# Kernel tuning notes

Measured on AMD Instinct MI355X. Metric: run time of the kernel, lower is better.

Reference implementation:

```python
import jax, jax.numpy as jnp
import numpy as np

HEADS = 4
HEAD_DIM = 32
DIM = 256
HIDDEN = HEADS * HEAD_DIM  # 128
SCALE = HEAD_DIM ** -0.5


def rmsnorm(x, g):
    # channel-wise L2 normalize (dim=1) * g * sqrt(C), lucidrains-style RMSNorm for conv maps
    inv = jax.lax.rsqrt(jnp.sum(x * x, axis=1, keepdims=True) + 1e-12)
    return x * inv * (g * (x.shape[1] ** 0.5))[None, :, None, None]


def setup_inputs() -> dict:
    key = jax.random.key(0)
    k1, k2, k3 = jax.random.split(key, 3)
    b, H, W = 16, 64, 64
    x = jax.random.normal(k1, (b, DIM, H, W), dtype=jnp.float32)
    W_qkv = jax.random.normal(k2, (3 * HIDDEN, DIM), dtype=jnp.float32) * (DIM ** -0.5)
    W_out = jax.random.normal(k3, (DIM, HIDDEN), dtype=jnp.float32) * (HIDDEN ** -0.5)
    b_out = jnp.zeros((DIM,), dtype=jnp.float32)
    g_norm = jnp.ones((DIM,), dtype=jnp.float32)
    g_out = jnp.ones((DIM,), dtype=jnp.float32)
    return {"x": x, "W_qkv": W_qkv, "W_out": W_out, "b_out": b_out,
            "g_norm": g_norm, "g_out": g_out}


def reference(x, W_qkv, W_out, b_out, g_norm, g_out):
    b, c, H, W = x.shape
    n = H * W
    xn = rmsnorm(x, g_norm)
    # 1x1 conv projection to q,k,v: (b, 3*hidden, H, W)
    qkv = jnp.einsum('bchw,oc->bohw', xn, W_qkv)
    qkv = qkv.reshape(b, 3, HEADS, HEAD_DIM, n)
    q, k, v = qkv[:, 0], qkv[:, 1], qkv[:, 2]  # (b, h, d, n)
    q = jax.nn.softmax(q, axis=-2)  # over head_dim
    k = jax.nn.softmax(k, axis=-1)  # over tokens
    # context: (b, h, d, e)
    context = jnp.einsum('bhdn,bhen->bhde', k, v)
    out = jnp.einsum('bhde,bhdn->bhen', context, q) * SCALE  # (b, h, e, n)
    out = out.reshape(b, HIDDEN, H, W)
    out = jnp.einsum('bchw,oc->bohw', out, W_out) + b_out[None, :, None, None]
    return rmsnorm(out, g_out)
```

## Files before the change

### kernel.cpp

```cpp
#include <hip/hip_runtime.h>


typedef _Float16 half8 __attribute__((ext_vector_type(8)));
typedef _Float16 half4 __attribute__((ext_vector_type(4)));
typedef float f32x4 __attribute__((ext_vector_type(4)));

#define SCALE_F 0.17677669529663687f

__global__ __launch_bounds__(256) void kW(const float* __restrict__ W_qkv,
                                          const float* __restrict__ W_out,
                                          const float* __restrict__ g_norm,
                                          _Float16* __restrict__ W16,
                                          _Float16* __restrict__ Wo16) {
  const int t = threadIdx.x;
  __shared__ float g16s[256];
  g16s[t] = g_norm[t] * 16.0f;
  __syncthreads();
  #pragma unroll
  for (int i = 0; i < 8; ++i) {
    int idx = blockIdx.x * 2048 + i * 256 + t;
    if (idx < 24576) {
      f32x4 v = *(const f32x4*)(W_qkv + (size_t)idx * 4);
      int c0 = (idx & 63) * 4;
      half4 h = {(_Float16)(v[0] * g16s[c0]), (_Float16)(v[1] * g16s[c0 + 1]),
                 (_Float16)(v[2] * g16s[c0 + 2]), (_Float16)(v[3] * g16s[c0 + 3])};
      *(half4*)(W16 + (size_t)idx * 4) = h;
    } else {
      f32x4 v = *(const f32x4*)(W_out + (size_t)(idx - 24576) * 4);
      half4 h = {(_Float16)v[0], (_Float16)v[1], (_Float16)v[2], (_Float16)v[3]};
      *(half4*)(Wo16 + (size_t)(idx - 24576) * 4) = h;
    }
  }
}

#define LOAD_AF(dst, mtv)                                                            \
  {                                                                                  \
    const _Float16* Wm_ = W16 + (size_t)((mtv) * 128 + h * 32) * 256;                \
    _Pragma("unroll")                                                                \
    for (int ks = 0; ks < 8; ++ks)                                                   \
      _Pragma("unroll")                                                              \
      for (int mf = 0; mf < 2; ++mf)                                                 \
        dst[ks][mf] = *(const half8*)(Wm_ + (size_t)(mf * 16 + ll) * 256 +           \
                                      ks * 32 + lg * 8);                             \
  }

#define GEMM_PHASE(afc)                                                              \
  {                                                                                  \
    _Pragma("unroll")                                                                \
    for (int i = 0; i < 2; ++i)                                                      \
      _Pragma("unroll")                                                              \
      for (int j = 0; j < 4; ++j) acc[i][j] = fz;                                    \
    _Pragma("unroll")                                                                \
    for (int ks = 0; ks < 8; ++ks) {                                                 \
      half8 bf[4];                                                                   \
      _Pragma("unroll")                                                              \
      for (int nf = 0; nf < 4; ++nf)                                                 \
        bf[nf] = *(const half8*)(xbuf + (nf * 16 + ll) * 512 +                       \
                                 ((((ks * 4 + lg) ^ ll) ^ ((nf & 1) << 4)) << 4));   \
      _Pragma("unroll")                                                              \
      for (int mf = 0; mf < 2; ++mf)                                                 \
        _Pragma("unroll")                                                            \
        for (int nf = 0; nf < 4; ++nf)                                               \
          acc[mf][nf] =                                                              \
              __builtin_amdgcn_mfma_f32_16x16x32_f16(afc[ks][mf], bf[nf],            \
                                                     acc[mf][nf], 0, 0, 0);          \
    }                                                                                \
  }

__global__ __launch_bounds__(256, 3) void k2_mega(const _Float16* __restrict__ W16,
                                                  const float* __restrict__ x,
                                                  _Float16* __restrict__ qhat,
                                                  float* __restrict__ ctxp,
                                                  float* __restrict__ sumep) {
  const int pt = blockIdx.x, b = blockIdx.y;
  const int p0 = pt * 64;
  const int t = threadIdx.x;
  const int h = t >> 6, l = t & 63;
  const int lg = l >> 4, ll = l & 15;
  const int u = l & 3;
  __shared__ __align__(1024) char smem[50432];
  char* xbuf = smem;
  char* r2 = smem + 32768;
  char* vt = smem;
  float* psum = (float*)(smem + 49152);
  float* sinvp = (float*)(smem + 50176);

  f32x4 vx[16];
  const float* xb = x + ((size_t)(b * 256 + h * 64)) * 4096 + p0 + (l & ~3);
  #pragma unroll
  for (int it = 0; it < 16; ++it)
    vx[it] = *(const f32x4*)(xb + (size_t)(it * 4 + u) * 4096);
  half8 afA[8][2], afB[8][2];
  LOAD_AF(afA, 0);
  float rsum = 0.f;
  #pragma unroll
  for (int it = 0; it < 16; ++it) {
    f32x4 v = vx[it];
    float sA = __shfl_xor((u & 1) ? v[0] : v[1], 1);
    float sB = __shfl_xor((u & 1) ? v[2] : v[3], 1);
    float a0 = (u & 1) ? sA : v[0];
    float a1 = (u & 1) ? v[1] : sA;
    float a2 = (u & 1) ? sB : v[2];
    float a3 = (u & 1) ? v[3] : sB;
    float sC = __shfl_xor((u & 2) ? a0 : a2, 2);
    float sD = __shfl_xor((u & 2) ? a1 : a3, 2);
    float w0 = (u & 2) ? sC : a0;
    float w1 = (u & 2) ? sD : a1;
    float w2 = (u & 2) ? a2 : sC;
    float w3 = (u & 2) ? a3 : sD;
    half4 hv = {(_Float16)w0, (_Float16)w1, (_Float16)w2, (_Float16)w3};
    #pragma unroll
    for (int j = 0; j < 4; ++j) { float f = (float)hv[j]; rsum += f * f; }
    int c = h * 8 + (it >> 1);
    int swz = c ^ (l & 15) ^ (((l >> 4) & 1) << 4);
    *(half4*)(xbuf + l * 512 + (swz << 4) + (it & 1) * 8) = hv;
  }
  psum[l * 4 + h] = rsum;
  __syncthreads();
  if (t < 64)
    sinvp[t] = rsqrtf(psum[t * 4] + psum[t * 4 + 1] + psum[t * 4 + 2] + psum[t * 4 + 3] + 1e-12f);
  __syncthreads();
  float sv[4];
  #pragma unroll
  for (int nf = 0; nf < 4; ++nf) sv[nf] = sinvp[nf * 16 + ll];

  const f32x4 fz = {0.f, 0.f, 0.f, 0.f};
  f32x4 acc[2][4];

  GEMM_PHASE(afA);
  LOAD_AF(afB, 1);
  {
    float s[4] = {0.f, 0.f, 0.f, 0.f};
    #pragma unroll
    for (int mf = 0; mf < 2; ++mf)
      #pragma unroll
      for (int nf = 0; nf < 4; ++nf)
        #pragma unroll
        for (int rr = 0; rr < 4; ++rr) {
          float v = __expf(acc[mf][nf][rr] * sv[nf]);
          acc[mf][nf][rr] = v;
          s[nf] += v;
        }
    #pragma unroll
    for (int nf = 0; nf < 4; ++nf) {
      s[nf] += __shfl_xor(s[nf], 16);
      s[nf] += __shfl_xor(s[nf], 32);
      s[nf] = 1.0f / s[nf];
    }
    #pragma unroll
    for (int mf = 0; mf < 2; ++mf)
      #pragma unroll
      for (int nf = 0; nf < 4; ++nf) {
        int px = nf * 16 + ll;
        int cphys = (h * 4 + mf * 2 + (lg >> 1)) ^ (px & 15);
        half4 hv;
        #pragma unroll
        for (int rr = 0; rr < 4; ++rr) hv[rr] = (_Float16)(acc[mf][nf][rr] * s[nf]);
        *(half4*)(r2 + px * 256 + (cphys << 4) + (lg & 1) * 8) = hv;
      }
    __syncthreads();
    _Float16* qb = qhat + ((size_t)b * 4096 + p0) * 128;
    #pragma unroll
    for (int i = 0; i < 4; ++i) {
      int q = i * 256 + t;
      int px = q >> 4, g = q & 15;
      half8 hv = *(const half8*)(r2 + px * 256 + ((g ^ (px & 15)) << 4));
      *(half8*)(qb + (size_t)px * 128 + g * 8) = hv;
    }
    __syncthreads();
  }

  GEMM_PHASE(afB);
  LOAD_AF(afA, 2);
  {
    float rs[2][4];
    #pragma unroll
    for (int mf = 0; mf < 2; ++mf)
      #pragma unroll
      for (int rr = 0; rr < 4; ++rr) rs[mf][rr] = 0.f;
    #pragma unroll
    for (int mf = 0; mf < 2; ++mf)
      #pragma unroll
      for (int nf = 0; nf < 4; ++nf)
        #pragma unroll
        for (int rr = 0; rr < 4; ++rr) {
          float v = __expf(acc[mf][nf][rr] * sv[nf] - 10.f);
          acc[mf][nf][rr] = v;
          rs[mf][rr] += v;
        }
    #pragma unroll
    for (int mf = 0; mf < 2; ++mf)
      #pragma unroll
      for (int rr = 0; rr < 4; ++rr) {
        float v = rs[mf][rr];
        v += __shfl_xor(v, 1);
        v += __shfl_xor(v, 2);
        v += __shfl_xor(v, 4);
        v += __shfl_xor(v, 8);
        rs[mf][rr] = v;
      }
    if (ll == 0) {
      #pragma unroll
      for (int mf = 0; mf < 2; ++mf)
        #pragma unroll
        for (int rr = 0; rr < 4; ++rr)
          sumep[((size_t)b * 128 + h * 32 + mf * 16 + lg * 4 + rr) * 64 + pt] = rs[mf][rr];
    }
    #pragma unroll
    for (int mf = 0; mf < 2; ++mf)
      #pragma unroll
      for (int nf = 0; nf < 4; ++nf)
        #pragma unroll
        for (int rr = 0; rr < 4; ++rr) {
          int ch = h * 32 + mf * 16 + lg * 4 + rr;
          int px = nf * 16 + ll;
          *(_Float16*)(r2 + ch * 128 + (((px >> 3) ^ (ch & 7)) << 4) + (px & 7) * 2) =
              (_Float16)acc[mf][nf][rr];
        }
  }

  GEMM_PHASE(afA);
  {
    __syncthreads();
    #pragma unroll
    for (int mf = 0; mf < 2; ++mf)
      #pragma unroll
      for (int nf = 0; nf < 4; ++nf)
        #pragma unroll
        for (int rr = 0; rr < 4; ++rr) {
          int ch = h * 32 + mf * 16 + lg * 4 + rr;
          int px = nf * 16 + ll;
          *(_Float16*)(vt + ch * 128 + (((px >> 3) ^ (ch & 7)) << 4) + (px & 7) * 2) =
              (_Float16)(acc[mf][nf][rr] * sv[nf]);
        }
    f32x4 ca[2][2] = {{fz, fz}, {fz, fz}};
    #pragma unroll
    for (int ks2 = 0; ks2 < 2; ++ks2) {
      half8 a2[2], b2[2];
      #pragma unroll
      for (int ti = 0; ti < 2; ++ti) {
        int ra = h * 32 + ti * 16 + ll;
        int cc = (ks2 * 4 + lg) ^ (ra & 7);
        a2[ti] = *(const half8*)(r2 + ra * 128 + (cc << 4));
        b2[ti] = *(const half8*)(vt + ra * 128 + (cc << 4));
      }
      #pragma unroll
      for (int ti = 0; ti < 2; ++ti)
        #pragma unroll
        for (int tj = 0; tj < 2; ++tj)
          ca[ti][tj] = __builtin_amdgcn_mfma_f32_16x16x32_f16(a2[ti], b2[tj], ca[ti][tj], 0, 0, 0);
    }
    float* cp = ctxp + (size_t)(((b * 64 + pt) * 4) + h) * 1024;
    #pragma unroll
    for (int ti = 0; ti < 2; ++ti)
      #pragma unroll
      for (int tj = 0; tj < 2; ++tj)
        #pragma unroll
        for (int rr = 0; rr < 4; ++rr)
          cp[(ti * 16 + lg * 4 + rr) * 32 + tj * 16 + ll] = ca[ti][tj][rr];
  }
}

__global__ __launch_bounds__(256) void k3_reduce(const float* __restrict__ ctxp,
                                                 const float* __restrict__ sumep,
                                                 float* __restrict__ ctx,
                                                 float* __restrict__ sume) {
  const int sl = blockIdx.x, b = blockIdx.y;
  const int t = threadIdx.x;
  if (sl == 0 && t < 128) {
    float s = 0.f;
    const float* sp = sumep + ((size_t)b * 128 + t) * 64;
    #pragma unroll 8
    for (int pt = 0; pt < 64; ++pt) s += sp[pt];
    sume[b * 128 + t] = s;
  }
  float a = 0.f;
  const float* p = ctxp + (size_t)b * 64 * 4096 + sl * 256 + t;
  #pragma unroll 8
  for (int pt = 0; pt < 64; ++pt) a += p[(size_t)pt * 4096];
  ctx[(size_t)b * 4096 + sl * 256 + t] = a;
}

__global__ __launch_bounds__(256) void k4b_fold(const _Float16* __restrict__ Wo16,
                                                const float* __restrict__ ctx,
                                                const float* __restrict__ sumexp,
                                                _Float16* __restrict__ M) {
  const int mq = blockIdx.x, b = blockIdx.y;
  const int t = threadIdx.x;
  const int h = t >> 6, l = t & 63;
  const int m0 = mq * 64;
  const float* cb = ctx + (size_t)(b * 4 + h) * 1024;
  const float* sb = sumexp + b * 128 + h * 32;
  half8 bf[2];
  #pragma unroll
  for (int n0 = 0; n0 < 2; ++n0) {
    int d = n0 * 16 + (l & 15);
    float s = SCALE_F / sb[d];
    const float* ce = cb + d * 32 + (l >> 4) * 8;
    half8 hb;
    #pragma unroll
    for (int j = 0; j < 8; ++j) hb[j] = (_Float16)(ce[j] * s);
    bf[n0] = hb;
  }
  const f32x4 fz = {0.f, 0.f, 0.f, 0.f};
  _Float16* Mb = M + (size_t)(b * 256) * 128;
  #pragma unroll
  for (int mf = 0; mf < 4; ++mf) {
    int row = m0 + mf * 16 + (l & 15);
    half8 af = *(const half8*)(Wo16 + (size_t)row * 128 + h * 32 + (l >> 4) * 8);
    #pragma unroll
    for (int n0 = 0; n0 < 2; ++n0) {
      f32x4 c = __builtin_amdgcn_mfma_f32_16x16x32_f16(af, bf[n0], fz, 0, 0, 0);
      #pragma unroll
      for (int rr = 0; rr < 4; ++rr) {
        int r = m0 + mf * 16 + (l >> 4) * 4 + rr;
        Mb[(size_t)r * 128 + h * 32 + n0 * 16 + (l & 15)] = (_Float16)c[rr];
      }
    }
  }
}

__global__ __launch_bounds__(256) void k5c_out(const _Float16* __restrict__ M,
                                               const _Float16* __restrict__ qhat,
                                               const float* __restrict__ b_out,
                                               const float* __restrict__ g_out,
                                               float* __restrict__ out) {
  const int pt = blockIdx.x, b = blockIdx.y;
  const int p0 = pt * 64;
  const int t = threadIdx.x;
  const int wid = t >> 6, l = t & 63;
  __shared__ __align__(16) char smem[81920];
  float* rp = (float*)smem;
  float* bo = (float*)(smem + 69632);
  float* g16o = (float*)(smem + 70656);
  float* psum = (float*)(smem + 71680);
  float* sinvp = (float*)(smem + 72704);
  const _Float16* Mb = M + (size_t)b * 256 * 128;
  const _Float16* Qb = qhat + ((size_t)b * 4096 + p0) * 128;
  #pragma unroll
  for (int i = 0; i < 16; ++i) {
    int ci = t + 256 * i;
    int r = ci >> 4, c = ci & 15;
    *(half8*)(smem + r * 256 + ((c ^ (r & 15)) << 4)) = *(const half8*)(Mb + (size_t)r * 128 + c * 8);
  }
  #pragma unroll
  for (int i = 0; i < 4; ++i) {
    int ci = t + 256 * i;
    int r = ci >> 4, c = ci & 15;
    *(half8*)(smem + 65536 + r * 256 + ((c ^ (r & 15)) << 4)) = *(const half8*)(Qb + (size_t)r * 128 + c * 8);
  }
  __syncthreads();
  const f32x4 fz = {0.f, 0.f, 0.f, 0.f};
  f32x4 acc[4][4];
  #pragma unroll
  for (int i = 0; i < 4; ++i)
    #pragma unroll
    for (int j = 0; j < 4; ++j) acc[i][j] = fz;
  #pragma unroll
  for (int kk = 0; kk < 4; ++kk) {
    half8 af[4], bf[4];
    int ck = kk * 4 + (l >> 4);
    #pragma unroll
    for (int mf = 0; mf < 4; ++mf) {
      int r = wid * 64 + mf * 16 + (l & 15);
      af[mf] = *(const half8*)(smem + r * 256 + ((ck ^ (r & 15)) << 4));
    }
    #pragma unroll
    for (int nf = 0; nf < 4; ++nf) {
      int r = nf * 16 + (l & 15);
      bf[nf] = *(const half8*)(smem + 65536 + r * 256 + ((ck ^ (r & 15)) << 4));
    }
    #pragma unroll
    for (int mf = 0; mf < 4; ++mf)
      #pragma unroll
      for (int nf = 0; nf < 4; ++nf)
        acc[mf][nf] = __builtin_amdgcn_mfma_f32_16x16x32_f16(af[mf], bf[nf], acc[mf][nf], 0, 0, 0);
  }
  __syncthreads();
  bo[t] = b_out[t];
  g16o[t] = g_out[t] * 16.0f;
  #pragma unroll
  for (int mf = 0; mf < 4; ++mf)
    #pragma unroll
    for (int nf = 0; nf < 4; ++nf)
      #pragma unroll
      for (int rr = 0; rr < 4; ++rr) {
        int r = wid * 64 + mf * 16 + (l >> 4) * 4 + rr;
        int px = nf * 16 + (l & 15);
        rp[r * 68 + px] = acc[mf][nf][rr];
      }
  __syncthreads();
  {
    int px = t & 63, q = t >> 6;
    float s = 0.f;
    #pragma unroll
    for (int i = 0; i < 64; ++i) {
      int r = q * 64 + i;
      float f = rp[r * 68 + px] + bo[r];
      s += f * f;
    }
    psum[px * 4 + q] = s;
  }
  __syncthreads();
  if (t < 64)
    sinvp[t] = rsqrtf(psum[t * 4] + psum[t * 4 + 1] + psum[t * 4 + 2] + psum[t * 4 + 3] + 1e-12f);
  __syncthreads();
  float* ob = out + (size_t)(b * 256) * 4096 + p0;
  #pragma unroll
  for (int i = 0; i < 16; ++i) {
    int idx4 = t + 256 * i;
    int r = idx4 >> 4, px4 = (idx4 & 15) * 4;
    f32x4 v;
    #pragma unroll
    for (int ii = 0; ii < 4; ++ii)
      v[ii] = (rp[r * 68 + px4 + ii] + bo[r]) * sinvp[px4 + ii] * g16o[r];
    *(f32x4*)(ob + (size_t)r * 4096 + px4) = v;
  }
}

extern "C" void kernel_launch(void* const* d_in, const int* in_sizes, int n_in,
                              void* d_out, int out_size, void* d_ws, size_t ws_size,
                              hipStream_t stream) {
  const float* x      = (const float*)d_in[0];
  const float* W_qkv  = (const float*)d_in[1];
  const float* W_out  = (const float*)d_in[2];
  const float* b_out  = (const float*)d_in[3];
  const float* g_norm = (const float*)d_in[4];
  const float* g_out  = (const float*)d_in[5];
  float* out = (float*)d_out;
  char* ws = (char*)d_ws;
  if (ws_size < 35659776) return;

  _Float16* W16   = (_Float16*)(ws);
  _Float16* Wo16  = (_Float16*)(ws + 196608);
  _Float16* qhat  = (_Float16*)(ws + 262144);
  float*    ctx   = (float*)(ws + 17039360);
  float*    sume  = (float*)(ws + 17301504);
  _Float16* M     = (_Float16*)(ws + 17309696);
  float*    ctxp  = (float*)(ws + 18358272);
  float*    sumep = (float*)(ws + 35135488);

  kW<<<16, 256, 0, stream>>>(W_qkv, W_out, g_norm, W16, Wo16);
  k2_mega<<<dim3(64, 16), 256, 0, stream>>>(W16, x, qhat, ctxp, sumep);
  k3_reduce<<<dim3(16, 16), 256, 0, stream>>>(ctxp, sumep, ctx, sume);
  k4b_fold<<<dim3(4, 16), 256, 0, stream>>>(Wo16, ctx, sume, M);
  k5c_out<<<dim3(64, 16), 256, 0, stream>>>(M, qhat, b_out, g_out, out);
}
```

Measured before the change: 77.86 us.

## Restructure QKV kernel: pixel-tiled waves with x fragments in registers, W streamed

The fused QKV/context kernel now gives each block 128 pixels and each wave 32 pixels. The normalized x fragments stay in registers as the MFMA A operand, and weights stream from global/L2 per output tile. The RMS norm is now computed per wave with shuffles, which removes the LDS staging of x and two block barriers. Query softmax results are written straight to global memory, and only k/v are staged in LDS for the context MFMA. Grid and partial-reduction counts are halved, at the cost of more per-wave global weight reads, lower occupancy (launch bounds 2) and scattered 2-byte qhat stores.

```diff
diff --git a/kernel.cpp b/kernel.cpp
--- a/kernel.cpp
+++ b/kernel.cpp
@@ -33,216 +33,166 @@
   }
 }
 
-#define LOAD_AF(dst, mtv)                                                            \
-  {                                                                                  \
-    const _Float16* Wm_ = W16 + (size_t)((mtv) * 128 + h * 32) * 256;                \
-    _Pragma("unroll")                                                                \
-    for (int ks = 0; ks < 8; ++ks)                                                   \
-      _Pragma("unroll")                                                              \
-      for (int mf = 0; mf < 2; ++mf)                                                 \
-        dst[ks][mf] = *(const half8*)(Wm_ + (size_t)(mf * 16 + ll) * 256 +           \
-                                      ks * 32 + lg * 8);                             \
-  }
-
-#define GEMM_PHASE(afc)                                                              \
-  {                                                                                  \
-    _Pragma("unroll")                                                                \
-    for (int i = 0; i < 2; ++i)                                                      \
-      _Pragma("unroll")                                                              \
-      for (int j = 0; j < 4; ++j) acc[i][j] = fz;                                    \
-    _Pragma("unroll")                                                                \
-    for (int ks = 0; ks < 8; ++ks) {                                                 \
-      half8 bf[4];                                                                   \
-      _Pragma("unroll")                                                              \
-      for (int nf = 0; nf < 4; ++nf)                                                 \
-        bf[nf] = *(const half8*)(xbuf + (nf * 16 + ll) * 512 +                       \
-                                 ((((ks * 4 + lg) ^ ll) ^ ((nf & 1) << 4)) << 4));   \
-      _Pragma("unroll")                                                              \
-      for (int mf = 0; mf < 2; ++mf)                                                 \
-        _Pragma("unroll")                                                            \
-        for (int nf = 0; nf < 4; ++nf)                                               \
-          acc[mf][nf] =                                                              \
-              __builtin_amdgcn_mfma_f32_16x16x32_f16(afc[ks][mf], bf[nf],            \
-                                                     acc[mf][nf], 0, 0, 0);          \
-    }                                                                                \
-  }
-
-__global__ __launch_bounds__(256, 3) void k2_mega(const _Float16* __restrict__ W16,
+__global__ __launch_bounds__(256, 2) void k2_mega(const _Float16* __restrict__ W16,
                                                   const float* __restrict__ x,
                                                   _Float16* __restrict__ qhat,
                                                   float* __restrict__ ctxp,
                                                   float* __restrict__ sumep) {
   const int pt = blockIdx.x, b = blockIdx.y;
-  const int p0 = pt * 64;
+  const int p0 = pt * 128;
   const int t = threadIdx.x;
-  const int h = t >> 6, l = t & 63;
+  const int w = t >> 6, l = t & 63;
   const int lg = l >> 4, ll = l & 15;
   const int u = l & 3;
-  __shared__ __align__(1024) char smem[50432];
-  char* xbuf = smem;
-  char* r2 = smem + 32768;
-  char* vt = smem;
-  float* psum = (float*)(smem + 49152);
-  float* sinvp = (float*)(smem + 50176);
-
-  f32x4 vx[16];
-  const float* xb = x + ((size_t)(b * 256 + h * 64)) * 4096 + p0 + (l & ~3);
-  #pragma unroll
-  for (int it = 0; it < 16; ++it)
-    vx[it] = *(const f32x4*)(xb + (size_t)(it * 4 + u) * 4096);
-  half8 afA[8][2], afB[8][2];
-  LOAD_AF(afA, 0);
-  float rsum = 0.f;
-  #pragma unroll
-  for (int it = 0; it < 16; ++it) {
-    f32x4 v = vx[it];
-    float sA = __shfl_xor((u & 1) ? v[0] : v[1], 1);
-    float sB = __shfl_xor((u & 1) ? v[2] : v[3], 1);
-    float a0 = (u & 1) ? sA : v[0];
-    float a1 = (u & 1) ? v[1] : sA;
-    float a2 = (u & 1) ? sB : v[2];
-    float a3 = (u & 1) ? v[3] : sB;
-    float sC = __shfl_xor((u & 2) ? a0 : a2, 2);
-    float sD = __shfl_xor((u & 2) ? a1 : a3, 2);
-    float w0 = (u & 2) ? sC : a0;
-    float w1 = (u & 2) ? sD : a1;
-    float w2 = (u & 2) ? a2 : sC;
-    float w3 = (u & 2) ? a3 : sD;
-    half4 hv = {(_Float16)w0, (_Float16)w1, (_Float16)w2, (_Float16)w3};
-    #pragma unroll
-    for (int j = 0; j < 4; ++j) { float f = (float)hv[j]; rsum += f * f; }
-    int c = h * 8 + (it >> 1);
-    int swz = c ^ (l & 15) ^ (((l >> 4) & 1) << 4);
-    *(half4*)(xbuf + l * 512 + (swz << 4) + (it & 1) * 8) = hv;
-  }
-  psum[l * 4 + h] = rsum;
-  __syncthreads();
-  if (t < 64)
-    sinvp[t] = rsqrtf(psum[t * 4] + psum[t * 4 + 1] + psum[t * 4 + 2] + psum[t * 4 + 3] + 1e-12f);
-  __syncthreads();
-  float sv[4];
-  #pragma unroll
-  for (int nf = 0; nf < 4; ++nf) sv[nf] = sinvp[nf * 16 + ll];
+  __shared__ __align__(1024) char smem[67584];
+  char* wt = smem;
+  char* vt = smem + 32768;
+  float* sums = (float*)(smem + 65536);
+
+  half8 af[2][8];
+  #pragma unroll
+  for (int s = 0; s < 2; ++s) {
+    const float* xb = x + ((size_t)b * 256) * 4096 + p0 + (2 * w + s) * 16 + ((l >> 2) & 3) * 4;
+    f32x4 tx[16];
+    #pragma unroll
+    for (int it = 0; it < 16; ++it) {
+      int ch = 32 * (it >> 1) + 8 * lg + 4 * (it & 1) + u;
+      f32x4 v = *(const f32x4*)(xb + (size_t)ch * 4096);
+      float sA = __shfl_xor((u & 1) ? v[0] : v[1], 1);
+      float sB = __shfl_xor((u & 1) ? v[2] : v[3], 1);
+      float a0 = (u & 1) ? sA : v[0];
+      float a1 = (u & 1) ? v[1] : sA;
+      float a2 = (u & 1) ? sB : v[2];
+      float a3 = (u & 1) ? v[3] : sB;
+      float sC = __shfl_xor((u & 2) ? a0 : a2, 2);
+      float sD = __shfl_xor((u & 2) ? a1 : a3, 2);
+      f32x4 o;
+      o[0] = (u & 2) ? sC : a0;
+      o[1] = (u & 2) ? sD : a1;
+      o[2] = (u & 2) ? a2 : sC;
+      o[3] = (u & 2) ? a3 : sD;
+      tx[it] = o;
+    }
+    float rs = 0.f;
+    #pragma unroll
+    for (int it = 0; it < 16; ++it)
+      #pragma unroll
+      for (int j = 0; j < 4; ++j) rs += tx[it][j] * tx[it][j];
+    rs += __shfl_xor(rs, 16);
+    rs += __shfl_xor(rs, 32);
+    float sinv = rsqrtf(rs + 1e-12f);
+    #pragma unroll
+    for (int ks = 0; ks < 8; ++ks) {
+      half8 hv;
+      #pragma unroll
+      for (int j = 0; j < 8; ++j)
+        hv[j] = (_Float16)(tx[ks * 2 + (j >> 2)][j & 3] * sinv);
+      af[s][ks] = hv;
+    }
+  }
 
   const f32x4 fz = {0.f, 0.f, 0.f, 0.f};
-  f32x4 acc[2][4];
-
-  GEMM_PHASE(afA);
-  LOAD_AF(afB, 1);
-  {
-    float s[4] = {0.f, 0.f, 0.f, 0.f};
-    #pragma unroll
-    for (int mf = 0; mf < 2; ++mf)
-      #pragma unroll
-      for (int nf = 0; nf < 4; ++nf)
-        #pragma unroll
-        for (int rr = 0; rr < 4; ++rr) {
-          float v = __expf(acc[mf][nf][rr] * sv[nf]);
-          acc[mf][nf][rr] = v;
-          s[nf] += v;
-        }
-    #pragma unroll
-    for (int nf = 0; nf < 4; ++nf) {
-      s[nf] += __shfl_xor(s[nf], 16);
-      s[nf] += __shfl_xor(s[nf], 32);
-      s[nf] = 1.0f / s[nf];
-    }
-    #pragma unroll
-    for (int mf = 0; mf < 2; ++mf)
-      #pragma unroll
-      for (int nf = 0; nf < 4; ++nf) {
-        int px = nf * 16 + ll;
-        int cphys = (h * 4 + mf * 2 + (lg >> 1)) ^ (px & 15);
-        half4 hv;
-        #pragma unroll
-        for (int rr = 0; rr < 4; ++rr) hv[rr] = (_Float16)(acc[mf][nf][rr] * s[nf]);
-        *(half4*)(r2 + px * 256 + (cphys << 4) + (lg & 1) * 8) = hv;
-      }
-    __syncthreads();
-    _Float16* qb = qhat + ((size_t)b * 4096 + p0) * 128;
-    #pragma unroll
-    for (int i = 0; i < 4; ++i) {
-      int q = i * 256 + t;
-      int px = q >> 4, g = q & 15;
-      half8 hv = *(const half8*)(r2 + px * 256 + ((g ^ (px & 15)) << 4));
-      *(half8*)(qb + (size_t)px * 128 + g * 8) = hv;
-    }
-    __syncthreads();
-  }
-
-  GEMM_PHASE(afB);
-  LOAD_AF(afA, 2);
-  {
-    float rs[2][4];
-    #pragma unroll
-    for (int mf = 0; mf < 2; ++mf)
-      #pragma unroll
-      for (int rr = 0; rr < 4; ++rr) rs[mf][rr] = 0.f;
-    #pragma unroll
-    for (int mf = 0; mf < 2; ++mf)
-      #pragma unroll
-      for (int nf = 0; nf < 4; ++nf)
-        #pragma unroll
-        for (int rr = 0; rr < 4; ++rr) {
-          float v = __expf(acc[mf][nf][rr] * sv[nf] - 10.f);
-          acc[mf][nf][rr] = v;
-          rs[mf][rr] += v;
-        }
-    #pragma unroll
-    for (int mf = 0; mf < 2; ++mf)
+  _Float16* qb = qhat + ((size_t)b * 4096 + p0) * 128;
+
+  #pragma unroll
+  for (int j = 0; j < 4; ++j) {
+    f32x4 a0[2] = {fz, fz}, a1[2] = {fz, fz};
+    #pragma unroll
+    for (int ks = 0; ks < 8; ++ks) {
+      half8 b0 = *(const half8*)(W16 + (size_t)(j * 32 + ll) * 256 + ks * 32 + lg * 8);
+      half8 b1 = *(const half8*)(W16 + (size_t)(j * 32 + 16 + ll) * 256 + ks * 32 + lg * 8);
+      #pragma unroll
+      for (int s = 0; s < 2; ++s) {
+        a0[s] = __builtin_amdgcn_mfma_f32_16x16x32_f16(af[s][ks], b0, a0[s], 0, 0, 0);
+        a1[s] = __builtin_amdgcn_mfma_f32_16x16x32_f16(af[s][ks], b1, a1[s], 0, 0, 0);
+      }
+    }
+    #pragma unroll
+    for (int s = 0; s < 2; ++s) {
+      float e0[4], e1[4], inv[4];
       #pragma unroll
       for (int rr = 0; rr < 4; ++rr) {
-        float v = rs[mf][rr];
+        e0[rr] = __expf(a0[s][rr]);
+        e1[rr] = __expf(a1[s][rr]);
+        float v = e0[rr] + e1[rr];
         v += __shfl_xor(v, 1);
         v += __shfl_xor(v, 2);
         v += __shfl_xor(v, 4);
         v += __shfl_xor(v, 8);
-        rs[mf][rr] = v;
-      }
-    if (ll == 0) {
-      #pragma unroll
-      for (int mf = 0; mf < 2; ++mf)
-        #pragma unroll
-        for (int rr = 0; rr < 4; ++rr)
-          sumep[((size_t)b * 128 + h * 32 + mf * 16 + lg * 4 + rr) * 64 + pt] = rs[mf][rr];
-    }
-    #pragma unroll
-    for (int mf = 0; mf < 2; ++mf)
-      #pragma unroll
-      for (int nf = 0; nf < 4; ++nf)
-        #pragma unroll
-        for (int rr = 0; rr < 4; ++rr) {
-          int ch = h * 32 + mf * 16 + lg * 4 + rr;
-          int px = nf * 16 + ll;
-          *(_Float16*)(r2 + ch * 128 + (((px >> 3) ^ (ch & 7)) << 4) + (px & 7) * 2) =
-              (_Float16)acc[mf][nf][rr];
-        }
-  }
-
-  GEMM_PHASE(afA);
+        inv[rr] = 1.0f / v;
+      }
+      #pragma unroll
+      for (int rr = 0; rr < 4; ++rr) {
+        int px = (2 * w + s) * 16 + lg * 4 + rr;
+        qb[(size_t)px * 128 + j * 32 + ll]      = (_Float16)(e0[rr] * inv[rr]);
+        qb[(size_t)px * 128 + j * 32 + 16 + ll] = (_Float16)(e1[rr] * inv[rr]);
+      }
+    }
+  }
+
+  #pragma unroll
+  for (int m = 0; m < 8; ++m) {
+    f32x4 a[2] = {fz, fz};
+    #pragma unroll
+    for (int ks = 0; ks < 8; ++ks) {
+      half8 bw = *(const half8*)(W16 + (size_t)(128 + m * 16 + ll) * 256 + ks * 32 + lg * 8);
+      #pragma unroll
+      for (int s = 0; s < 2; ++s)
+        a[s] = __builtin_amdgcn_mfma_f32_16x16x32_f16(af[s][ks], bw, a[s], 0, 0, 0);
+    }
+    int row = m * 16 + ll;
+    float part = 0.f;
+    #pragma unroll
+    for (int s = 0; s < 2; ++s) {
+      half4 hv;
+      #pragma unroll
+      for (int rr = 0; rr < 4; ++rr) {
+        float e = __expf(a[s][rr] - 10.f);
+        part += e;
+        hv[rr] = (_Float16)e;
+      }
+      int c = (2 * w + s) * 2 + (lg >> 1);
+      *(half4*)(wt + row * 256 + ((c ^ (row & 15)) << 4) + (lg & 1) * 8) = hv;
+    }
+    part += __shfl_xor(part, 16);
+    part += __shfl_xor(part, 32);
+    if (lg == 0) sums[row * 4 + w] = part;
+  }
+
+  #pragma unroll
+  for (int m = 0; m < 8; ++m) {
+    f32x4 a[2] = {fz, fz};
+    #pragma unroll
+    for (int ks = 0; ks < 8; ++ks) {
+      half8 bw = *(const half8*)(W16 + (size_t)(256 + m * 16 + ll) * 256 + ks * 32 + lg * 8);
+      #pragma unroll
+      for (int s = 0; s < 2; ++s)
+        a[s] = __builtin_amdgcn_mfma_f32_16x16x32_f16(af[s][ks], bw, a[s], 0, 0, 0);
+    }
+    int row = m * 16 + ll;
+    #pragma unroll
+    for (int s = 0; s < 2; ++s) {
+      half4 hv;
+      #pragma unroll
+      for (int rr = 0; rr < 4; ++rr) hv[rr] = (_Float16)a[s][rr];
+      int c = (2 * w + s) * 2 + (lg >> 1);
+      *(half4*)(vt + row * 256 + ((c ^ (row & 15)) << 4) + (lg & 1) * 8) = hv;
+    }
+  }
+
+  __syncthreads();
+
   {
-    __syncthreads();
-    #pragma unroll
-    for (int mf = 0; mf < 2; ++mf)
-      #pragma unroll
-      for (int nf = 0; nf < 4; ++nf)
-        #pragma unroll
-        for (int rr = 0; rr < 4; ++rr) {
-          int ch = h * 32 + mf * 16 + lg * 4 + rr;
-          int px = nf * 16 + ll;
-          *(_Float16*)(vt + ch * 128 + (((px >> 3) ^ (ch & 7)) << 4) + (px & 7) * 2) =
-              (_Float16)(acc[mf][nf][rr] * sv[nf]);
-        }
     f32x4 ca[2][2] = {{fz, fz}, {fz, fz}};
     #pragma unroll
-    for (int ks2 = 0; ks2 < 2; ++ks2) {
+    for (int ks2 = 0; ks2 < 4; ++ks2) {
       half8 a2[2], b2[2];
       #pragma unroll
       for (int ti = 0; ti < 2; ++ti) {
-        int ra = h * 32 + ti * 16 + ll;
-        int cc = (ks2 * 4 + lg) ^ (ra & 7);
-        a2[ti] = *(const half8*)(r2 + ra * 128 + (cc << 4));
-        b2[ti] = *(const half8*)(vt + ra * 128 + (cc << 4));
+        int row = w * 32 + ti * 16 + ll;
+        int c = (ks2 * 4 + lg) ^ (row & 15);
+        a2[ti] = *(const half8*)(wt + row * 256 + (c << 4));
+        b2[ti] = *(const half8*)(vt + row * 256 + (c << 4));
       }
       #pragma unroll
       for (int ti = 0; ti < 2; ++ti)
@@ -250,7 +200,7 @@
         for (int tj = 0; tj < 2; ++tj)
           ca[ti][tj] = __builtin_amdgcn_mfma_f32_16x16x32_f16(a2[ti], b2[tj], ca[ti][tj], 0, 0, 0);
     }
-    float* cp = ctxp + (size_t)(((b * 64 + pt) * 4) + h) * 1024;
+    float* cp = ctxp + (size_t)(((b * 32 + pt) * 4) + w) * 1024;
     #pragma unroll
     for (int ti = 0; ti < 2; ++ti)
       #pragma unroll
@@ -258,6 +208,14 @@
         #pragma unroll
         for (int rr = 0; rr < 4; ++rr)
           cp[(ti * 16 + lg * 4 + rr) * 32 + tj * 16 + ll] = ca[ti][tj][rr];
+    if (lg == 0) {
+      #pragma unroll
+      for (int ti = 0; ti < 2; ++ti) {
+        int ch = w * 32 + ti * 16 + ll;
+        float s4 = sums[ch * 4] + sums[ch * 4 + 1] + sums[ch * 4 + 2] + sums[ch * 4 + 3];
+        sumep[((size_t)b * 128 + ch) * 32 + pt] = s4;
+      }
+    }
   }
 }
 
@@ -269,15 +227,15 @@
   const int t = threadIdx.x;
   if (sl == 0 && t < 128) {
     float s = 0.f;
-    const float* sp = sumep + ((size_t)b * 128 + t) * 64;
+    const float* sp = sumep + ((size_t)b * 128 + t) * 32;
     #pragma unroll 8
-    for (int pt = 0; pt < 64; ++pt) s += sp[pt];
+    for (int pt = 0; pt < 32; ++pt) s += sp[pt];
     sume[b * 128 + t] = s;
   }
   float a = 0.f;
-  const float* p = ctxp + (size_t)b * 64 * 4096 + sl * 256 + t;
+  const float* p = ctxp + (size_t)b * 32 * 4096 + sl * 256 + t;
   #pragma unroll 8
-  for (int pt = 0; pt < 64; ++pt) a += p[(size_t)pt * 4096];
+  for (int pt = 0; pt < 32; ++pt) a += p[(size_t)pt * 4096];
   ctx[(size_t)b * 4096 + sl * 256 + t] = a;
 }
 
@@ -441,7 +399,7 @@
   float*    sumep = (float*)(ws + 35135488);
 
   kW<<<16, 256, 0, stream>>>(W_qkv, W_out, g_norm, W16, Wo16);
-  k2_mega<<<dim3(64, 16), 256, 0, stream>>>(W16, x, qhat, ctxp, sumep);
+  k2_mega<<<dim3(32, 16), 256, 0, stream>>>(W16, x, qhat, ctxp, sumep);
   k3_reduce<<<dim3(16, 16), 256, 0, stream>>>(ctxp, sumep, ctx, sume);
   k4b_fold<<<dim3(4, 16), 256, 0, stream>>>(Wo16, ctx, sume, M);
   k5c_out<<<dim3(64, 16), 256, 0, stream>>>(M, qhat, b_out, g_out, out);
```

Result: slower. 99.22 us (+27.4%).

## Halve k2 pixel tile to 32 and double grid, raising occupancy

Applied to the files above, without the earlier changes.

Halves the pixel tile of the fused QKV-projection kernel from 64 to 32 and doubles its grid to 128x16 blocks. Shared memory drops and launch bounds rise to 4 blocks per CU, and a single weight-fragment buffer replaces the double buffer to free registers. The x-load mapping, the LDS layouts and the context MFMA (now a single k-step) are reworked to match. In exchange, the per-tile partial context and sum-exp buffers double, so the reduction kernel reads twice as many partials and the workspace grows.

```diff
diff --git a/kernel.cpp b/kernel.cpp
--- a/kernel.cpp
+++ b/kernel.cpp
@@ -49,53 +49,55 @@
     _Pragma("unroll")                                                                \
     for (int i = 0; i < 2; ++i)                                                      \
       _Pragma("unroll")                                                              \
-      for (int j = 0; j < 4; ++j) acc[i][j] = fz;                                    \
+      for (int j = 0; j < 2; ++j) acc[i][j] = fz;                                    \
     _Pragma("unroll")                                                                \
     for (int ks = 0; ks < 8; ++ks) {                                                 \
-      half8 bf[4];                                                                   \
+      half8 bf[2];                                                                   \
       _Pragma("unroll")                                                              \
-      for (int nf = 0; nf < 4; ++nf)                                                 \
+      for (int nf = 0; nf < 2; ++nf)                                                 \
         bf[nf] = *(const half8*)(xbuf + (nf * 16 + ll) * 512 +                       \
-                                 ((((ks * 4 + lg) ^ ll) ^ ((nf & 1) << 4)) << 4));   \
+                                 ((((ks * 4 + lg) ^ ll) ^ (nf << 4)) << 4));         \
       _Pragma("unroll")                                                              \
       for (int mf = 0; mf < 2; ++mf)                                                 \
         _Pragma("unroll")                                                            \
-        for (int nf = 0; nf < 4; ++nf)                                               \
+        for (int nf = 0; nf < 2; ++nf)                                               \
           acc[mf][nf] =                                                              \
               __builtin_amdgcn_mfma_f32_16x16x32_f16(afc[ks][mf], bf[nf],            \
                                                      acc[mf][nf], 0, 0, 0);          \
     }                                                                                \
   }
 
-__global__ __launch_bounds__(256, 3) void k2_mega(const _Float16* __restrict__ W16,
+__global__ __launch_bounds__(256, 4) void k2_mega(const _Float16* __restrict__ W16,
                                                   const float* __restrict__ x,
                                                   _Float16* __restrict__ qhat,
                                                   float* __restrict__ ctxp,
                                                   float* __restrict__ sumep) {
   const int pt = blockIdx.x, b = blockIdx.y;
-  const int p0 = pt * 64;
+  const int p0 = pt * 32;
   const int t = threadIdx.x;
   const int h = t >> 6, l = t & 63;
   const int lg = l >> 4, ll = l & 15;
-  const int u = l & 3;
-  __shared__ __align__(1024) char smem[50432];
+  const int u = l & 3, pq = (l >> 2) & 7, hi = l >> 5;
+  __shared__ __align__(1024) char smem[37504];
   char* xbuf = smem;
-  char* r2 = smem + 32768;
-  char* vt = smem;
-  float* psum = (float*)(smem + 49152);
-  float* sinvp = (float*)(smem + 50176);
-
-  f32x4 vx[16];
-  const float* xb = x + ((size_t)(b * 256 + h * 64)) * 4096 + p0 + (l & ~3);
-  #pragma unroll
-  for (int it = 0; it < 16; ++it)
-    vx[it] = *(const f32x4*)(xb + (size_t)(it * 4 + u) * 4096);
-  half8 afA[8][2], afB[8][2];
-  LOAD_AF(afA, 0);
+  char* r2 = smem + 16384;
+  char* vt = smem + 26624;
+  float* psum = (float*)(smem + 36864);
+  float* sinvp = (float*)(smem + 37376);
+
+  f32x4 tx[8];
+  const float* xb = x + ((size_t)b * 256) * 4096 + p0 + pq * 4;
+  #pragma unroll
+  for (int it = 0; it < 8; ++it) {
+    int ch = h * 64 + it * 8 + hi * 4 + u;
+    tx[it] = *(const f32x4*)(xb + (size_t)ch * 4096);
+  }
+  half8 af[8][2];
+  LOAD_AF(af, 0);
   float rsum = 0.f;
   #pragma unroll
-  for (int it = 0; it < 16; ++it) {
-    f32x4 v = vx[it];
+  for (int it = 0; it < 8; ++it) {
+    f32x4 v = tx[it];
     float sA = __shfl_xor((u & 1) ? v[0] : v[1], 1);
     float sB = __shfl_xor((u & 1) ? v[2] : v[3], 1);
     float a0 = (u & 1) ? sA : v[0];
@@ -111,30 +113,32 @@
     half4 hv = {(_Float16)w0, (_Float16)w1, (_Float16)w2, (_Float16)w3};
     #pragma unroll
     for (int j = 0; j < 4; ++j) { float f = (float)hv[j]; rsum += f * f; }
-    int c = h * 8 + (it >> 1);
-    int swz = c ^ (l & 15) ^ (((l >> 4) & 1) << 4);
-    *(half4*)(xbuf + l * 512 + (swz << 4) + (it & 1) * 8) = hv;
-  }
-  psum[l * 4 + h] = rsum;
-  __syncthreads();
-  if (t < 64)
+    int px = pq * 4 + u;
+    int c = h * 8 + it;
+    int swz = c ^ (px & 15) ^ (((px >> 4) & 1) << 4);
+    *(half4*)(xbuf + px * 512 + (swz << 4) + hi * 8) = hv;
+  }
+  rsum += __shfl_xor(rsum, 32);
+  if (l < 32) psum[l * 4 + h] = rsum;
+  __syncthreads();
+  if (t < 32)
     sinvp[t] = rsqrtf(psum[t * 4] + psum[t * 4 + 1] + psum[t * 4 + 2] + psum[t * 4 + 3] + 1e-12f);
   __syncthreads();
-  float sv[4];
-  #pragma unroll
-  for (int nf = 0; nf < 4; ++nf) sv[nf] = sinvp[nf * 16 + ll];
+  float sv[2];
+  #pragma unroll
+  for (int nf = 0; nf < 2; ++nf) sv[nf] = sinvp[nf * 16 + ll];
 
   const f32x4 fz = {0.f, 0.f, 0.f, 0.f};
-  f32x4 acc[2][4];
-
-  GEMM_PHASE(afA);
-  LOAD_AF(afB, 1);
+  f32x4 acc[2][2];
+
+  GEMM_PHASE(af);
+  LOAD_AF(af, 1);
   {
-    float s[4] = {0.f, 0.f, 0.f, 0.f};
-    #pragma unroll
-    for (int mf = 0; mf < 2; ++mf)
-      #pragma unroll
-      for (int nf = 0; nf < 4; ++nf)
+    float s[2] = {0.f, 0.f};
+    #pragma unroll
+    for (int mf = 0; mf < 2; ++mf)
+      #pragma unroll
+      for (int nf = 0; nf < 2; ++nf)
         #pragma unroll
         for (int rr = 0; rr < 4; ++rr) {
           float v = __expf(acc[mf][nf][rr] * sv[nf]);
@@ -142,7 +146,7 @@
           s[nf] += v;
         }
     #pragma unroll
-    for (int nf = 0; nf < 4; ++nf) {
+    for (int nf = 0; nf < 2; ++nf) {
       s[nf] += __shfl_xor(s[nf], 16);
       s[nf] += __shfl_xor(s[nf], 32);
       s[nf] = 1.0f / s[nf];
@@ -150,7 +154,7 @@
     #pragma unroll
     for (int mf = 0; mf < 2; ++mf)
       #pragma unroll
-      for (int nf = 0; nf < 4; ++nf) {
+      for (int nf = 0; nf < 2; ++nf) {
         int px = nf * 16 + ll;
         int cphys = (h * 4 + mf * 2 + (lg >> 1)) ^ (px & 15);
         half4 hv;
@@ -161,7 +165,7 @@
     __syncthreads();
     _Float16* qb = qhat + ((size_t)b * 4096 + p0) * 128;
     #pragma unroll
-    for (int i = 0; i < 4; ++i) {
+    for (int i = 0; i < 2; ++i) {
       int q = i * 256 + t;
       int px = q >> 4, g = q & 15;
       half8 hv = *(const half8*)(r2 + px * 256 + ((g ^ (px & 15)) << 4));
@@ -170,8 +174,8 @@
     __syncthreads();
   }
 
-  GEMM_PHASE(afB);
-  LOAD_AF(afA, 2);
+  GEMM_PHASE(af);
+  LOAD_AF(af, 2);
   {
     float rs[2][4];
     #pragma unroll
@@ -181,7 +185,7 @@
     #pragma unroll
     for (int mf = 0; mf < 2; ++mf)
       #pragma unroll
-      for (int nf = 0; nf < 4; ++nf)
+      for (int nf = 0; nf < 2; ++nf)
         #pragma unroll
         for (int rr = 0; rr < 4; ++rr) {
           float v = __expf(acc[mf][nf][rr] * sv[nf] - 10.f);
@@ -204,53 +208,46 @@
       for (int mf = 0; mf < 2; ++mf)
         #pragma unroll
         for (int rr = 0; rr < 4; ++rr)
-          sumep[((size_t)b * 128 + h * 32 + mf * 16 + lg * 4 + rr) * 64 + pt] = rs[mf][rr];
-    }
-    #pragma unroll
-    for (int mf = 0; mf < 2; ++mf)
-      #pragma unroll
-      for (int nf = 0; nf < 4; ++nf)
+          sumep[((size_t)b * 128 + h * 32 + mf * 16 + lg * 4 + rr) * 128 + pt] = rs[mf][rr];
+    }
+    #pragma unroll
+    for (int mf = 0; mf < 2; ++mf)
+      #pragma unroll
+      for (int nf = 0; nf < 2; ++nf)
         #pragma unroll
         for (int rr = 0; rr < 4; ++rr) {
           int ch = h * 32 + mf * 16 + lg * 4 + rr;
           int px = nf * 16 + ll;
-          *(_Float16*)(r2 + ch * 128 + (((px >> 3) ^ (ch & 7)) << 4) + (px & 7) * 2) =
-              (_Float16)acc[mf][nf][rr];
+          *(_Float16*)(r2 + ch * 80 + px * 2) = (_Float16)acc[mf][nf][rr];
         }
   }
 
-  GEMM_PHASE(afA);
+  GEMM_PHASE(af);
   {
-    __syncthreads();
-    #pragma unroll
-    for (int mf = 0; mf < 2; ++mf)
-      #pragma unroll
-      for (int nf = 0; nf < 4; ++nf)
+    #pragma unroll
+    for (int mf = 0; mf < 2; ++mf)
+      #pragma unroll
+      for (int nf = 0; nf < 2; ++nf)
         #pragma unroll
         for (int rr = 0; rr < 4; ++rr) {
           int ch = h * 32 + mf * 16 + lg * 4 + rr;
           int px = nf * 16 + ll;
-          *(_Float16*)(vt + ch * 128 + (((px >> 3) ^ (ch & 7)) << 4) + (px & 7) * 2) =
-              (_Float16)(acc[mf][nf][rr] * sv[nf]);
+          *(_Float16*)(vt + ch * 80 + px * 2) = (_Float16)(acc[mf][nf][rr] * sv[nf]);
         }
-    f32x4 ca[2][2] = {{fz, fz}, {fz, fz}};
-    #pragma unroll
-    for (int ks2 = 0; ks2 < 2; ++ks2) {
-      half8 a2[2], b2[2];
-      #pragma unroll
-      for (int ti = 0; ti < 2; ++ti) {
-        int ra = h * 32 + ti * 16 + ll;
-        int cc = (ks2 * 4 + lg) ^ (ra & 7);
-        a2[ti] = *(const half8*)(r2 + ra * 128 + (cc << 4));
-        b2[ti] = *(const half8*)(vt + ra * 128 + (cc << 4));
-      }
-      #pragma unroll
-      for (int ti = 0; ti < 2; ++ti)
-        #pragma unroll
-        for (int tj = 0; tj < 2; ++tj)
-          ca[ti][tj] = __builtin_amdgcn_mfma_f32_16x16x32_f16(a2[ti], b2[tj], ca[ti][tj], 0, 0, 0);
-    }
-    float* cp = ctxp + (size_t)(((b * 64 + pt) * 4) + h) * 1024;
+    f32x4 ca[2][2];
+    half8 a2[2], b2[2];
+    #pragma unroll
+    for (int ti = 0; ti < 2; ++ti) {
+      int row = h * 32 + ti * 16 + ll;
+      a2[ti] = *(const half8*)(r2 + row * 80 + lg * 16);
+      b2[ti] = *(const half8*)(vt + row * 80 + lg * 16);
+    }
+    #pragma unroll
+    for (int ti = 0; ti < 2; ++ti)
+      #pragma unroll
+      for (int tj = 0; tj < 2; ++tj)
+        ca[ti][tj] = __builtin_amdgcn_mfma_f32_16x16x32_f16(a2[ti], b2[tj], fz, 0, 0, 0);
+    float* cp = ctxp + (size_t)(((b * 128 + pt) * 4) + h) * 1024;
     #pragma unroll
     for (int ti = 0; ti < 2; ++ti)
       #pragma unroll
@@ -269,15 +266,15 @@
   const int t = threadIdx.x;
   if (sl == 0 && t < 128) {
     float s = 0.f;
-    const float* sp = sumep + ((size_t)b * 128 + t) * 64;
+    const float* sp = sumep + ((size_t)b * 128 + t) * 128;
     #pragma unroll 8
-    for (int pt = 0; pt < 64; ++pt) s += sp[pt];
+    for (int pt = 0; pt < 128; ++pt) s += sp[pt];
     sume[b * 128 + t] = s;
   }
   float a = 0.f;
-  const float* p = ctxp + (size_t)b * 64 * 4096 + sl * 256 + t;
+  const float* p = ctxp + (size_t)b * 128 * 4096 + sl * 256 + t;
   #pragma unroll 8
-  for (int pt = 0; pt < 64; ++pt) a += p[(size_t)pt * 4096];
+  for (int pt = 0; pt < 128; ++pt) a += p[(size_t)pt * 4096];
   ctx[(size_t)b * 4096 + sl * 256 + t] = a;
 }
 
@@ -429,7 +426,7 @@
   const float* g_out  = (const float*)d_in[5];
   float* out = (float*)d_out;
   char* ws = (char*)d_ws;
-  if (ws_size < 35659776) return;
+  if (ws_size < 52961280) return;
 
   _Float16* W16   = (_Float16*)(ws);
   _Float16* Wo16  = (_Float16*)(ws + 196608);
@@ -438,10 +435,10 @@
   float*    sume  = (float*)(ws + 17301504);
   _Float16* M     = (_Float16*)(ws + 17309696);
   float*    ctxp  = (float*)(ws + 18358272);
-  float*    sumep = (float*)(ws + 35135488);
+  float*    sumep = (float*)(ws + 51912704);
 
   kW<<<16, 256, 0, stream>>>(W_qkv, W_out, g_norm, W16, Wo16);
-  k2_mega<<<dim3(64, 16), 256, 0, stream>>>(W16, x, qhat, ctxp, sumep);
+  k2_mega<<<dim3(128, 16), 256, 0, stream>>>(W16, x, qhat, ctxp, sumep);
   k3_reduce<<<dim3(16, 16), 256, 0, stream>>>(ctxp, sumep, ctx, sume);
   k4b_fold<<<dim3(4, 16), 256, 0, stream>>>(Wo16, ctx, sume, M);
   k5c_out<<<dim3(64, 16), 256, 0, stream>>>(M, qhat, b_out, g_out, out);
```

Measured after the change: 104.1 us. 1.34x slower.

## Fuse partial-context reduction into fold kernel and write q directly to global

Applied to the files above, without the earlier changes.

Merges the k3 reduction of per-tile context/sum partials into the k4b fold kernel, so each (head,batch) block reduces its own slice into shared memory before the MFMA fold. This drops one launch and the ctx/sume round trip through global memory. In k2_mega the q-hat output is now stored straight from registers as half4 writes instead of being staged through shared memory with two barriers, and each thread computes the rsqrt normalization itself rather than going through an extra barrier. The risks are less coalesced q stores and a reduction spread over only 64 blocks, which cuts parallelism for the 16 MB ctxp read.

```diff
diff --git a/kernel.cpp b/kernel.cpp
--- a/kernel.cpp
+++ b/kernel.cpp
@@ -78,12 +78,11 @@
   const int h = t >> 6, l = t & 63;
   const int lg = l >> 4, ll = l & 15;
   const int u = l & 3;
-  __shared__ __align__(1024) char smem[50432];
+  __shared__ __align__(1024) char smem[50176];
   char* xbuf = smem;
-  char* r2 = smem + 32768;
+  char* wt = smem + 32768;
   char* vt = smem;
   float* psum = (float*)(smem + 49152);
-  float* sinvp = (float*)(smem + 50176);
 
   f32x4 vx[16];
   const float* xb = x + ((size_t)(b * 256 + h * 64)) * 4096 + p0 + (l & ~3);
@@ -117,12 +116,13 @@
   }
   psum[l * 4 + h] = rsum;
   __syncthreads();
-  if (t < 64)
-    sinvp[t] = rsqrtf(psum[t * 4] + psum[t * 4 + 1] + psum[t * 4 + 2] + psum[t * 4 + 3] + 1e-12f);
-  __syncthreads();
   float sv[4];
   #pragma unroll
-  for (int nf = 0; nf < 4; ++nf) sv[nf] = sinvp[nf * 16 + ll];
+  for (int nf = 0; nf < 4; ++nf) {
+    int px = nf * 16 + ll;
+    sv[nf] = rsqrtf(psum[px * 4] + psum[px * 4 + 1] + psum[px * 4 + 2] +
+                    psum[px * 4 + 3] + 1e-12f);
+  }
 
   const f32x4 fz = {0.f, 0.f, 0.f, 0.f};
   f32x4 acc[2][4];
@@ -147,27 +147,17 @@
       s[nf] += __shfl_xor(s[nf], 32);
       s[nf] = 1.0f / s[nf];
     }
+    _Float16* qb = qhat + ((size_t)b * 4096 + p0) * 128 + h * 32 + lg * 4;
     #pragma unroll
     for (int mf = 0; mf < 2; ++mf)
       #pragma unroll
       for (int nf = 0; nf < 4; ++nf) {
         int px = nf * 16 + ll;
-        int cphys = (h * 4 + mf * 2 + (lg >> 1)) ^ (px & 15);
         half4 hv;
         #pragma unroll
         for (int rr = 0; rr < 4; ++rr) hv[rr] = (_Float16)(acc[mf][nf][rr] * s[nf]);
-        *(half4*)(r2 + px * 256 + (cphys << 4) + (lg & 1) * 8) = hv;
+        *(half4*)(qb + (size_t)px * 128 + mf * 16) = hv;
       }
-    __syncthreads();
-    _Float16* qb = qhat + ((size_t)b * 4096 + p0) * 128;
-    #pragma unroll
-    for (int i = 0; i < 4; ++i) {
-      int q = i * 256 + t;
-      int px = q >> 4, g = q & 15;
-      half8 hv = *(const half8*)(r2 + px * 256 + ((g ^ (px & 15)) << 4));
-      *(half8*)(qb + (size_t)px * 128 + g * 8) = hv;
-    }
-    __syncthreads();
   }
 
   GEMM_PHASE(afB);
@@ -214,7 +204,7 @@
         for (int rr = 0; rr < 4; ++rr) {
           int ch = h * 32 + mf * 16 + lg * 4 + rr;
           int px = nf * 16 + ll;
-          *(_Float16*)(r2 + ch * 128 + (((px >> 3) ^ (ch & 7)) << 4) + (px & 7) * 2) =
+          *(_Float16*)(wt + ch * 128 + (((px >> 3) ^ (ch & 7)) << 4) + (px & 7) * 2) =
               (_Float16)acc[mf][nf][rr];
         }
   }
@@ -241,7 +231,7 @@
       for (int ti = 0; ti < 2; ++ti) {
         int ra = h * 32 + ti * 16 + ll;
         int cc = (ks2 * 4 + lg) ^ (ra & 7);
-        a2[ti] = *(const half8*)(r2 + ra * 128 + (cc << 4));
+        a2[ti] = *(const half8*)(wt + ra * 128 + (cc << 4));
         b2[ti] = *(const half8*)(vt + ra * 128 + (cc << 4));
       }
       #pragma unroll
@@ -261,42 +251,40 @@
   }
 }
 
-__global__ __launch_bounds__(256) void k3_reduce(const float* __restrict__ ctxp,
-                                                 const float* __restrict__ sumep,
-                                                 float* __restrict__ ctx,
-                                                 float* __restrict__ sume) {
-  const int sl = blockIdx.x, b = blockIdx.y;
+__global__ __launch_bounds__(256) void k34(const float* __restrict__ ctxp,
+                                           const float* __restrict__ sumep,
+                                           const _Float16* __restrict__ Wo16,
+                                           _Float16* __restrict__ M) {
+  const int h = blockIdx.x, b = blockIdx.y;
   const int t = threadIdx.x;
-  if (sl == 0 && t < 128) {
+  __shared__ float ctx_s[1024];
+  __shared__ float sis[32];
+  {
+    f32x4 a = {0.f, 0.f, 0.f, 0.f};
+    const float* p = ctxp + ((size_t)(b * 64) * 4 + h) * 1024 + t * 4;
+    #pragma unroll 8
+    for (int pt = 0; pt < 64; ++pt) {
+      f32x4 v = *(const f32x4*)(p + (size_t)pt * 4096);
+      a[0] += v[0]; a[1] += v[1]; a[2] += v[2]; a[3] += v[3];
+    }
+    *(f32x4*)(ctx_s + t * 4) = a;
+  }
+  if (t < 32) {
     float s = 0.f;
-    const float* sp = sumep + ((size_t)b * 128 + t) * 64;
+    const float* sp = sumep + ((size_t)b * 128 + h * 32 + t) * 64;
     #pragma unroll 8
     for (int pt = 0; pt < 64; ++pt) s += sp[pt];
-    sume[b * 128 + t] = s;
-  }
-  float a = 0.f;
-  const float* p = ctxp + (size_t)b * 64 * 4096 + sl * 256 + t;
-  #pragma unroll 8
-  for (int pt = 0; pt < 64; ++pt) a += p[(size_t)pt * 4096];
-  ctx[(size_t)b * 4096 + sl * 256 + t] = a;
-}
-
-__global__ __launch_bounds__(256) void k4b_fold(const _Float16* __restrict__ Wo16,
-                                                const float* __restrict__ ctx,
-                                                const float* __restrict__ sumexp,
-                                                _Float16* __restrict__ M) {
-  const int mq = blockIdx.x, b = blockIdx.y;
-  const int t = threadIdx.x;
-  const int h = t >> 6, l = t & 63;
-  const int m0 = mq * 64;
-  const float* cb = ctx + (size_t)(b * 4 + h) * 1024;
-  const float* sb = sumexp + b * 128 + h * 32;
+    sis[t] = SCALE_F / s;
+  }
+  __syncthreads();
+  const int w = t >> 6, l = t & 63;
+  const int m0 = w * 64;
   half8 bf[2];
   #pragma unroll
   for (int n0 = 0; n0 < 2; ++n0) {
     int d = n0 * 16 + (l & 15);
-    float s = SCALE_F / sb[d];
-    const float* ce = cb + d * 32 + (l >> 4) * 8;
+    float s = sis[d];
+    const float* ce = ctx_s + d * 32 + (l >> 4) * 8;
     half8 hb;
     #pragma unroll
     for (int j = 0; j < 8; ++j) hb[j] = (_Float16)(ce[j] * s);
@@ -434,15 +422,12 @@
   _Float16* W16   = (_Float16*)(ws);
   _Float16* Wo16  = (_Float16*)(ws + 196608);
   _Float16* qhat  = (_Float16*)(ws + 262144);
-  float*    ctx   = (float*)(ws + 17039360);
-  float*    sume  = (float*)(ws + 17301504);
-  _Float16* M     = (_Float16*)(ws + 17309696);
+  _Float16* M     = (_Float16*)(ws + 17039360);
   float*    ctxp  = (float*)(ws + 18358272);
   float*    sumep = (float*)(ws + 35135488);
 
   kW<<<16, 256, 0, stream>>>(W_qkv, W_out, g_norm, W16, Wo16);
   k2_mega<<<dim3(64, 16), 256, 0, stream>>>(W16, x, qhat, ctxp, sumep);
-  k3_reduce<<<dim3(16, 16), 256, 0, stream>>>(ctxp, sumep, ctx, sume);
-  k4b_fold<<<dim3(4, 16), 256, 0, stream>>>(Wo16, ctx, sume, M);
+  k34<<<dim3(4, 16), 256, 0, stream>>>(ctxp, sumep, Wo16, M);
   k5c_out<<<dim3(64, 16), 256, 0, stream>>>(M, qhat, b_out, g_out, out);
 }
```

Measured after the change: 78.86 us. About the same (+1.3%).
